# Performance work log

Measured on AMD Instinct MI355X. Metric: run time of the kernel, lower is better.

The kernel has to match this reference:

```python
import jax, jax.numpy as jnp
import numpy as np

H, D, BS = 32, 128, 16  # num heads, head dim, paged-KV block size
ROPE_BASE = 10000.0
NEG_INF = -1e30


def setup_inputs() -> dict:
    key = jax.random.key(0)
    ks = jax.random.split(key, 8)
    B, KV, hidden = 8, 2048, H * D  # decode: one new token per sequence
    max_blocks = KV // BS
    num_slots = B * KV

    hidden_states = jax.random.normal(ks[0], (B, hidden), jnp.float32) * 0.02

    # rotary cos/sin for the current position of each sequence (pos = KV-1)
    inv_freq = 1.0 / (ROPE_BASE ** (jnp.arange(0, D, 2, dtype=jnp.float32) / D))
    pos = jnp.full((B,), KV - 1, jnp.float32)
    ang = pos[:, None] * inv_freq[None, :]            # [B, D/2]
    cos, sin = jnp.cos(ang), jnp.sin(ang)

    w_qkv = jax.random.normal(ks[1], (3 * H * D, hidden), jnp.float32) * 0.02
    b_qkv = jax.random.normal(ks[2], (3 * H * D,), jnp.float32) * 0.02
    w_o = jax.random.normal(ks[3], (hidden, H * D), jnp.float32) * 0.02

    k_cache = jax.random.normal(ks[4], (num_slots, H, D), jnp.float32) * 0.5
    v_cache = jax.random.normal(ks[5], (num_slots, H, D), jnp.float32) * 0.5

    # contiguous block allocation: seq b owns blocks [b*max_blocks, (b+1)*max_blocks)
    block_tables = jnp.arange(B * max_blocks, dtype=jnp.int32).reshape(B, max_blocks)
    slots = (jnp.arange(B, dtype=jnp.int32) * KV + (KV - 1)).astype(jnp.int32)
    input_lengths = jnp.full((B,), KV, jnp.int32)

    return dict(hidden_states=hidden_states, cos=cos, sin=sin,
                w_qkv=w_qkv, b_qkv=b_qkv, w_o=w_o,
                k_cache=k_cache, v_cache=v_cache,
                block_tables=block_tables, slots=slots,
                input_lengths=input_lengths, max_s=KV)


def _rope(x, cos, sin):
    # flash-attn style (non-interleaved) rotary: split head dim in halves
    x1, x2 = jnp.split(x, 2, axis=-1)                 # [T, H, D/2] each
    c, s = cos[:, None, :], sin[:, None, :]
    return jnp.concatenate([x1 * c - x2 * s, x1 * s + x2 * c], axis=-1)


def reference(hidden_states, cos, sin, w_qkv, b_qkv, w_o,
              k_cache, v_cache, block_tables, slots, input_lengths, max_s):
    B = hidden_states.shape[0]
    # fused QKV projection (c_attn, bias=True)
    qkv = hidden_states @ w_qkv.T + b_qkv             # [B, 3*H*D]
    q, k, v = jnp.split(qkv, 3, axis=1)
    q = q.reshape(B, H, D)
    k = k.reshape(B, H, D)
    v = v.reshape(B, H, D)

    # rotary applied in-place to q and k[:,0] in the original
    q = _rope(q, cos, sin)
    k = _rope(k, cos, sin)

    # reshape_and_cache: scatter current k/v into the paged KV cache
    k_cache = k_cache.at[slots].set(k)
    v_cache = v_cache.at[slots].set(v)

    # paged_attn: gather KV via block tables, masked softmax over valid length
    pos = jnp.arange(max_s)                           # [S]
    idx = block_tables[:, pos // BS] * BS + (pos % BS)[None, :]  # [B, S] slot ids
    keys = k_cache[idx]                               # [B, S, H, D]
    vals = v_cache[idx]                               # [B, S, H, D]

    scale = D ** -0.5
    scores = jnp.einsum('bhd,bshd->bhs', q, keys) * scale
    valid = pos[None, :] < input_lengths[:, None]     # [B, S]
    scores = jnp.where(valid[:, None, :], scores, NEG_INF)
    probs = jax.nn.softmax(scores, axis=-1)
    attn = jnp.einsum('bhs,bshd->bhd', probs, vals)   # [B, H, D]

    # o_proj (c_proj, bias=False)
    return attn.reshape(B, H * D) @ w_o.T
```

## Files before the change

kernel.cpp:

```cpp
#include <hip/hip_runtime.h>

#define NH 32
#define HD 128
#define PBS 16
#define HIDDEN (NH * HD)
#define QKVN (3 * HIDDEN)
#define NSPLIT 8

__global__ __launch_bounds__(256) void gemv4r(const float* __restrict__ x,
                                              const float* __restrict__ W,
                                              const float* __restrict__ bias,
                                              float* __restrict__ out,
                                              int N, int K) {
    const int lane = threadIdx.x & 63;
    const int wv   = (blockIdx.x * blockDim.x + threadIdx.x) >> 6;
    const int n0   = wv * 4;
    if (n0 >= N) return;
    const float* w0 = W + (size_t)n0 * K;

    float acc[4][8];
#pragma unroll
    for (int r = 0; r < 4; ++r)
#pragma unroll
        for (int b = 0; b < 8; ++b) acc[r][b] = 0.f;

#pragma unroll 2
    for (int k0 = lane * 4; k0 < K; k0 += 256) {
        float4 w4[4];
#pragma unroll
        for (int r = 0; r < 4; ++r)
            w4[r] = *reinterpret_cast<const float4*>(w0 + (size_t)r * K + k0);
#pragma unroll
        for (int b = 0; b < 8; ++b) {
            const float4 x4 = *reinterpret_cast<const float4*>(x + (size_t)b * K + k0);
#pragma unroll
            for (int r = 0; r < 4; ++r)
                acc[r][b] += w4[r].x * x4.x + w4[r].y * x4.y +
                             w4[r].z * x4.z + w4[r].w * x4.w;
        }
    }
#pragma unroll
    for (int r = 0; r < 4; ++r)
#pragma unroll
        for (int b = 0; b < 8; ++b)
#pragma unroll
            for (int off = 32; off > 0; off >>= 1)
                acc[r][b] += __shfl_xor(acc[r][b], off, 64);
    if (lane == 0) {
#pragma unroll
        for (int r = 0; r < 4; ++r) {
            const float bv = bias ? bias[n0 + r] : 0.f;
#pragma unroll
            for (int b = 0; b < 8; ++b)
                out[(size_t)b * N + n0 + r] = acc[r][b] + bv;
        }
    }
}

__global__ __launch_bounds__(256) void rope_k(float* __restrict__ qkv,
                                              const float* __restrict__ cosb,
                                              const float* __restrict__ sinb,
                                              int B) {
    const int tid = blockIdx.x * blockDim.x + threadIdx.x;
    const int total = 2 * B * NH * (HD / 2);
    if (tid >= total) return;
    const int d = tid % (HD / 2);
    const int h = (tid / (HD / 2)) % NH;
    const int b = (tid / (HD / 2) / NH) % B;
    const int part = tid / (HD / 2) / NH / B;
    const float c = cosb[b * (HD / 2) + d];
    const float s = sinb[b * (HD / 2) + d];
    float* p = qkv + (size_t)b * QKVN + part * HIDDEN + h * HD + d;
    const float x1 = p[0];
    const float x2 = p[HD / 2];
    p[0]      = x1 * c - x2 * s;
    p[HD / 2] = x1 * s + x2 * c;
}

__global__ __launch_bounds__(256) void attn_part(const float* __restrict__ qkv,
                                                 const float* __restrict__ k_cache,
                                                 const float* __restrict__ v_cache,
                                                 const int* __restrict__ block_tables,
                                                 const int* __restrict__ slots,
                                                 const int* __restrict__ lengths,
                                                 float* __restrict__ part_o,
                                                 float* __restrict__ part_ml,
                                                 int S, int max_blocks) {
    const int split = blockIdx.x % NSPLIT;
    const int bh    = blockIdx.x / NSPLIT;
    const int b     = bh >> 5;
    const int h     = bh & 31;
    const int SP    = S / NSPLIT;
    const int base  = split * SP;

    extern __shared__ float smem[];
    float* sc    = smem;
    int*   bt    = (int*)(smem + SP);
    float* red   = smem + SP + SP / PBS;
    float* stage = red + 16;

    const int tid  = threadIdx.x;
    const int lane = tid & 63;
    const int wid  = tid >> 6;
    const int nw   = blockDim.x >> 6;
    const int half = lane >> 5;
    const int l32  = lane & 31;

    const int nbt = SP / PBS;
    for (int i = tid; i < nbt; i += blockDim.x)
        bt[i] = block_tables[b * max_blocks + base / PBS + i];
    __syncthreads();

    const int slot_b = slots[b];
    const int len    = lengths[b];
    const float scale = 0.088388347648318447f;

    const float* qp   = qkv + (size_t)b * QKVN + h * HD;
    const float* newk = qkv + (size_t)b * QKVN + HIDDEN + h * HD;
    const float* newv = qkv + (size_t)b * QKVN + 2 * HIDDEN + h * HD;
    const float4 q4 = *reinterpret_cast<const float4*>(qp + l32 * 4);

    const int STEP = nw * 16;
    for (int s0 = wid * 16; s0 < SP; s0 += STEP) {
        float4 k4[8];
#pragma unroll
        for (int u = 0; u < 8; ++u) {
            const int p = s0 + u * 2 + half;
            const int idx = bt[p >> 4] * PBS + (p & (PBS - 1));
            const float* kp = (idx == slot_b) ? newk
                                              : (k_cache + (size_t)idx * HIDDEN + h * HD);
            k4[u] = *reinterpret_cast<const float4*>(kp + l32 * 4);
        }
#pragma unroll
        for (int u = 0; u < 8; ++u) {
            const int p = s0 + u * 2 + half;
            float d = k4[u].x * q4.x + k4[u].y * q4.y + k4[u].z * q4.z + k4[u].w * q4.w;
#pragma unroll
            for (int off = 16; off > 0; off >>= 1) d += __shfl_xor(d, off, 64);
            if (l32 == 0) sc[p] = (base + p < len) ? d * scale : -1e30f;
        }
    }
    __syncthreads();

    float m = -1e30f;
    for (int s = tid; s < SP; s += blockDim.x) m = fmaxf(m, sc[s]);
#pragma unroll
    for (int off = 32; off > 0; off >>= 1) m = fmaxf(m, __shfl_xor(m, off, 64));
    if (lane == 0) red[wid] = m;
    __syncthreads();
    float bm = red[0];
    for (int w = 1; w < nw; ++w) bm = fmaxf(bm, red[w]);
    __syncthreads();

    float lsum = 0.f;
    for (int s = tid; s < SP; s += blockDim.x) {
        const float e = __expf(sc[s] - bm);
        sc[s] = e;
        lsum += e;
    }
#pragma unroll
    for (int off = 32; off > 0; off >>= 1) lsum += __shfl_xor(lsum, off, 64);
    if (lane == 0) red[wid] = lsum;
    __syncthreads();
    float tot = 0.f;
    for (int w = 0; w < nw; ++w) tot += red[w];

    float4 acc[8];
#pragma unroll
    for (int u = 0; u < 8; ++u) acc[u] = make_float4(0.f, 0.f, 0.f, 0.f);
    for (int s0 = wid * 16; s0 < SP; s0 += STEP) {
        float4 v4[8];
        float pr[8];
#pragma unroll
        for (int u = 0; u < 8; ++u) {
            const int p = s0 + u * 2 + half;
            const int idx = bt[p >> 4] * PBS + (p & (PBS - 1));
            const float* vp = (idx == slot_b) ? newv
                                              : (v_cache + (size_t)idx * HIDDEN + h * HD);
            v4[u] = *reinterpret_cast<const float4*>(vp + l32 * 4);
            pr[u] = sc[p];
        }
#pragma unroll
        for (int u = 0; u < 8; ++u) {
            acc[u].x += pr[u] * v4[u].x;
            acc[u].y += pr[u] * v4[u].y;
            acc[u].z += pr[u] * v4[u].z;
            acc[u].w += pr[u] * v4[u].w;
        }
    }
    float4 a = acc[0];
#pragma unroll
    for (int u = 1; u < 8; ++u) {
        a.x += acc[u].x; a.y += acc[u].y; a.z += acc[u].z; a.w += acc[u].w;
    }
    a.x += __shfl_xor(a.x, 32, 64);
    a.y += __shfl_xor(a.y, 32, 64);
    a.z += __shfl_xor(a.z, 32, 64);
    a.w += __shfl_xor(a.w, 32, 64);

    if (half == 0)
        *reinterpret_cast<float4*>(&stage[wid * HD + l32 * 4]) = a;
    __syncthreads();
    if (wid == 0) {
        float t0 = 0.f, t1 = 0.f;
        for (int w = 0; w < nw; ++w) {
            t0 += stage[w * HD + lane * 2];
            t1 += stage[w * HD + lane * 2 + 1];
        }
        float* po = part_o + ((size_t)bh * NSPLIT + split) * HD;
        po[lane * 2]     = t0;
        po[lane * 2 + 1] = t1;
        if (lane == 0) {
            part_ml[((size_t)bh * NSPLIT + split) * 2]     = bm;
            part_ml[((size_t)bh * NSPLIT + split) * 2 + 1] = tot;
        }
    }
}

__global__ __launch_bounds__(HD) void attn_reduce(const float* __restrict__ part_o,
                                                  const float* __restrict__ part_ml,
                                                  float* __restrict__ attn_out) {
    const int bh = blockIdx.x;
    const int d  = threadIdx.x;
    float M = -1e30f;
#pragma unroll
    for (int i = 0; i < NSPLIT; ++i)
        M = fmaxf(M, part_ml[((size_t)bh * NSPLIT + i) * 2]);
    float L = 0.f, o = 0.f;
#pragma unroll
    for (int i = 0; i < NSPLIT; ++i) {
        const float mi = part_ml[((size_t)bh * NSPLIT + i) * 2];
        const float li = part_ml[((size_t)bh * NSPLIT + i) * 2 + 1];
        const float w  = __expf(mi - M);
        L += li * w;
        o += part_o[((size_t)bh * NSPLIT + i) * HD + d] * w;
    }
    attn_out[(size_t)bh * HD + d] = o / L;
}

extern "C" void kernel_launch(void* const* d_in, const int* in_sizes, int n_in,
                              void* d_out, int out_size, void* d_ws, size_t ws_size,
                              hipStream_t stream) {
    const float* hidden  = (const float*)d_in[0];
    const float* cosb    = (const float*)d_in[1];
    const float* sinb    = (const float*)d_in[2];
    const float* w_qkv   = (const float*)d_in[3];
    const float* b_qkv   = (const float*)d_in[4];
    const float* w_o     = (const float*)d_in[5];
    const float* k_cache = (const float*)d_in[6];
    const float* v_cache = (const float*)d_in[7];
    const int*   btab    = (const int*)d_in[8];
    const int*   slots   = (const int*)d_in[9];
    const int*   lens    = (const int*)d_in[10];

    const int B = in_sizes[0] / HIDDEN;
    const int max_blocks = in_sizes[8] / B;
    const int S = max_blocks * PBS;

    float* qkv     = (float*)d_ws;
    float* attn    = qkv + (size_t)B * QKVN;
    float* part_o  = attn + (size_t)B * HIDDEN;
    float* part_ml = part_o + (size_t)B * NH * NSPLIT * HD;
    float* out     = (float*)d_out;

    gemv4r<<<QKVN / 16, 256, 0, stream>>>(hidden, w_qkv, b_qkv, qkv, QKVN, HIDDEN);

    {
        const int total = 2 * B * NH * (HD / 2);
        rope_k<<<(total + 255) / 256, 256, 0, stream>>>(qkv, cosb, sinb, B);
    }

    {
        const int SP = S / NSPLIT;
        const size_t smem = (size_t)(SP + SP / PBS + 16 + 4 * HD) * sizeof(float);
        attn_part<<<B * NH * NSPLIT, 256, smem, stream>>>(qkv, k_cache, v_cache,
                                                          btab, slots, lens,
                                                          part_o, part_ml, S, max_blocks);
        attn_reduce<<<B * NH, HD, 0, stream>>>(part_o, part_ml, attn);
    }

    gemv4r<<<HIDDEN / 16, 256, 0, stream>>>(attn, w_o, nullptr, out, HIDDEN, HIDDEN);
}
```

Baseline: 205.7 us.

## Remap attention lanes so each 4-lane group handles one token per page

The K and V loops in attn_part now assign a whole 16-token page to each wavefront. Each group of four lanes handles one token and reads the full 128-float head row in strided float4 chunks. This replaces the old scheme, where each half-wavefront covered one token per unrolled step and needed a five-step shuffle reduction per token. The dot product now needs only two shuffles, and the block-table lookup happens once per page instead of once per token. The cost is an extra q register footprint, a larger shuffle reduction of the V accumulators at the end, and a different memory access pattern within each wavefront.

After: 217.3 us. 1.06x slower.

```diff
diff --git a/kernel.cpp b/kernel.cpp
--- a/kernel.cpp
+++ b/kernel.cpp
@@ -92,22 +92,22 @@
     const int h     = bh & 31;
     const int SP    = S / NSPLIT;
     const int base  = split * SP;
+    const int NPG   = SP / PBS;
 
     extern __shared__ float smem[];
     float* sc    = smem;
     int*   bt    = (int*)(smem + SP);
-    float* red   = smem + SP + SP / PBS;
+    float* red   = smem + SP + NPG;
     float* stage = red + 16;
 
     const int tid  = threadIdx.x;
     const int lane = tid & 63;
     const int wid  = tid >> 6;
     const int nw   = blockDim.x >> 6;
-    const int half = lane >> 5;
-    const int l32  = lane & 31;
-
-    const int nbt = SP / PBS;
-    for (int i = tid; i < nbt; i += blockDim.x)
+    const int t16  = lane >> 2;
+    const int qi   = lane & 3;
+
+    for (int i = tid; i < NPG; i += blockDim.x)
         bt[i] = block_tables[b * max_blocks + base / PBS + i];
     __syncthreads();
 
@@ -116,28 +116,32 @@
     const float scale = 0.088388347648318447f;
 
     const float* qp   = qkv + (size_t)b * QKVN + h * HD;
-    const float* newk = qkv + (size_t)b * QKVN + HIDDEN + h * HD;
-    const float* newv = qkv + (size_t)b * QKVN + 2 * HIDDEN + h * HD;
-    const float4 q4 = *reinterpret_cast<const float4*>(qp + l32 * 4);
-
-    const int STEP = nw * 16;
-    for (int s0 = wid * 16; s0 < SP; s0 += STEP) {
+    const float* newk = qp + HIDDEN;
+    const float* newv = qp + 2 * HIDDEN;
+
+    float4 qf[8];
+#pragma unroll
+    for (int u = 0; u < 8; ++u)
+        qf[u] = *reinterpret_cast<const float4*>(qp + u * 16 + qi * 4);
+
+    for (int pg = wid; pg < NPG; pg += nw) {
+        const int idx = bt[pg] * PBS + t16;
+        const float* kp = (idx == slot_b) ? newk
+                                          : (k_cache + (size_t)idx * HIDDEN + h * HD);
         float4 k4[8];
 #pragma unroll
-        for (int u = 0; u < 8; ++u) {
-            const int p = s0 + u * 2 + half;
-            const int idx = bt[p >> 4] * PBS + (p & (PBS - 1));
-            const float* kp = (idx == slot_b) ? newk
-                                              : (k_cache + (size_t)idx * HIDDEN + h * HD);
-            k4[u] = *reinterpret_cast<const float4*>(kp + l32 * 4);
-        }
-#pragma unroll
-        for (int u = 0; u < 8; ++u) {
-            const int p = s0 + u * 2 + half;
-            float d = k4[u].x * q4.x + k4[u].y * q4.y + k4[u].z * q4.z + k4[u].w * q4.w;
-#pragma unroll
-            for (int off = 16; off > 0; off >>= 1) d += __shfl_xor(d, off, 64);
-            if (l32 == 0) sc[p] = (base + p < len) ? d * scale : -1e30f;
+        for (int u = 0; u < 8; ++u)
+            k4[u] = *reinterpret_cast<const float4*>(kp + u * 16 + qi * 4);
+        float d = 0.f;
+#pragma unroll
+        for (int u = 0; u < 8; ++u)
+            d += k4[u].x * qf[u].x + k4[u].y * qf[u].y +
+                 k4[u].z * qf[u].z + k4[u].w * qf[u].w;
+        d += __shfl_xor(d, 1, 64);
+        d += __shfl_xor(d, 2, 64);
+        if (qi == 0) {
+            const int ploc = pg * PBS + t16;
+            sc[ploc] = (base + ploc < len) ? d * scale : -1e30f;
         }
     }
     __syncthreads();
@@ -168,38 +172,38 @@
     float4 acc[8];
 #pragma unroll
     for (int u = 0; u < 8; ++u) acc[u] = make_float4(0.f, 0.f, 0.f, 0.f);
-    for (int s0 = wid * 16; s0 < SP; s0 += STEP) {
+    for (int pg = wid; pg < NPG; pg += nw) {
+        const int idx = bt[pg] * PBS + t16;
+        const float* vp = (idx == slot_b) ? newv
+                                          : (v_cache + (size_t)idx * HIDDEN + h * HD);
         float4 v4[8];
-        float pr[8];
+#pragma unroll
+        for (int u = 0; u < 8; ++u)
+            v4[u] = *reinterpret_cast<const float4*>(vp + u * 16 + qi * 4);
+        const float pt = sc[pg * PBS + t16];
 #pragma unroll
         for (int u = 0; u < 8; ++u) {
-            const int p = s0 + u * 2 + half;
-            const int idx = bt[p >> 4] * PBS + (p & (PBS - 1));
-            const float* vp = (idx == slot_b) ? newv
-                                              : (v_cache + (size_t)idx * HIDDEN + h * HD);
-            v4[u] = *reinterpret_cast<const float4*>(vp + l32 * 4);
-            pr[u] = sc[p];
-        }
-#pragma unroll
-        for (int u = 0; u < 8; ++u) {
-            acc[u].x += pr[u] * v4[u].x;
-            acc[u].y += pr[u] * v4[u].y;
-            acc[u].z += pr[u] * v4[u].z;
-            acc[u].w += pr[u] * v4[u].w;
-        }
-    }
-    float4 a = acc[0];
-#pragma unroll
-    for (int u = 1; u < 8; ++u) {
-        a.x += acc[u].x; a.y += acc[u].y; a.z += acc[u].z; a.w += acc[u].w;
-    }
-    a.x += __shfl_xor(a.x, 32, 64);
-    a.y += __shfl_xor(a.y, 32, 64);
-    a.z += __shfl_xor(a.z, 32, 64);
-    a.w += __shfl_xor(a.w, 32, 64);
-
-    if (half == 0)
-        *reinterpret_cast<float4*>(&stage[wid * HD + l32 * 4]) = a;
+            acc[u].x += pt * v4[u].x;
+            acc[u].y += pt * v4[u].y;
+            acc[u].z += pt * v4[u].z;
+            acc[u].w += pt * v4[u].w;
+        }
+    }
+#pragma unroll
+    for (int u = 0; u < 8; ++u) {
+#pragma unroll
+        for (int off = 4; off <= 32; off <<= 1) {
+            acc[u].x += __shfl_xor(acc[u].x, off, 64);
+            acc[u].y += __shfl_xor(acc[u].y, off, 64);
+            acc[u].z += __shfl_xor(acc[u].z, off, 64);
+            acc[u].w += __shfl_xor(acc[u].w, off, 64);
+        }
+    }
+    if (t16 == 0) {
+#pragma unroll
+        for (int u = 0; u < 8; ++u)
+            *reinterpret_cast<float4*>(&stage[wid * HD + u * 16 + qi * 4]) = acc[u];
+    }
     __syncthreads();
     if (wid == 0) {
         float t0 = 0.f, t1 = 0.f;
```
